# Kernel optimization log

Measured on AMD Instinct MI355X. Metric: run time of the kernel, lower is better.

Reference implementation:

```python
import jax, jax.numpy as jnp
import numpy as np

EPS = 1e-5

def prelu(x, a):
    return jnp.where(x >= 0, x, a * x)

def batch_norm(x, axes):
    # training-mode BatchNorm with gamma=1, beta=0 (init values)
    m = jnp.mean(x, axis=axes, keepdims=True)
    v = jnp.var(x, axis=axes, keepdims=True)
    return (x - m) / jnp.sqrt(v + EPS)

def conv_branch(X, w, b):
    # X: [B,N,F]; Conv2d(1,1,(1,k)) over the feature axis, VALID
    lhs = X[:, None, :, :]                      # [B,1,N,F]
    rhs = w.reshape(1, 1, 1, -1)                # OIHW
    out = jax.lax.conv_general_dilated(lhs, rhs, (1, 1), 'VALID',
        dimension_numbers=('NCHW', 'OIHW', 'NCHW'))
    return out[:, 0] + b                        # [B,N,F-k+1]

def setup_inputs() -> dict:
    key = jax.random.key(0)
    ks = jax.random.split(key, 16)
    B, N, F, H, D = 8192, 29, 147, 4, 128
    d_cat = 429
    s = 0.05
    return {
        'X': jax.random.normal(ks[0], (B, N, F), jnp.float32),
        'corr': jax.random.uniform(ks[1], (B, N, N), jnp.float32),
        'w_c1': s * jax.random.normal(ks[2], (3,), jnp.float32),
        'b_c1': jnp.zeros((1,), jnp.float32),
        'w_c2': s * jax.random.normal(ks[3], (5,), jnp.float32),
        'b_c2': jnp.zeros((1,), jnp.float32),
        'w_c3': s * jax.random.normal(ks[4], (7,), jnp.float32),
        'b_c3': jnp.zeros((1,), jnp.float32),
        'a_cnn': 0.25 * jnp.ones((1,), jnp.float32),
        'Wg': s * jax.random.normal(ks[5], (d_cat, D), jnp.float32),
        'bg': jnp.zeros((D,), jnp.float32),
        'a_gnn': 0.25 * jnp.ones((1,), jnp.float32),
        'centroids': jax.random.normal(ks[6], (H, 1, D), jnp.float32),
        'head_w': s * jax.random.normal(ks[7], (H,), jnp.float32),
        'Wp': s * jax.random.normal(ks[8], (D, D), jnp.float32),
        'bp': jnp.zeros((D,), jnp.float32),
        'Wm1': s * jax.random.normal(ks[9], (D, D), jnp.float32),
        'bm1': jnp.zeros((D,), jnp.float32),
        'a_mlp': 0.25 * jnp.ones((1,), jnp.float32),
        'Wm2': s * jax.random.normal(ks[10], (D, 1), jnp.float32),
        'bm2': jnp.zeros((1,), jnp.float32),
    }

def reference(X, corr, w_c1, b_c1, w_c2, b_c2, w_c3, b_c3, a_cnn,
              Wg, bg, a_gnn, centroids, head_w, Wp, bp,
              Wm1, bm1, a_mlp, Wm2, bm2):
    # three conv branches + concat + PReLU + BN over node channels
    a1 = conv_branch(X, w_c1, b_c1)             # [B,29,145]
    a2 = conv_branch(X, w_c2, b_c2)             # [B,29,143]
    a3 = conv_branch(X, w_c3, b_c3)             # [B,29,141]
    x = prelu(jnp.concatenate([a1, a2, a3], axis=2), a_cnn)  # [B,29,429]
    x = batch_norm(x, (0, 2))
    # GraphConv: A x W + b
    x = jnp.einsum('bnm,bmd->bnd', corr, x) @ Wg + bg        # [B,29,128]
    x = prelu(x, a_gnn)
    x = batch_norm(x, (0, 2))
    # CoSimPool: multi-head cosine-sim attention assignment to 1 cluster
    xn = x / (jnp.linalg.norm(x, axis=-1, keepdims=True) + 1e-8)
    cn = centroids / (jnp.linalg.norm(centroids, axis=-1, keepdims=True) + 1e-8)
    sim = jnp.einsum('hmd,bnd->bhmn', cn, xn)                # [B,4,1,29]
    agg = jnp.einsum('h,bhmn->bmn', head_w, sim)             # 1x1 conv over heads
    C = jax.nn.softmax(agg, axis=-1)                         # [B,1,29]
    x = jnp.einsum('bmn,bnd->bmd', C, x) @ Wp + bp           # [B,1,128]
    x = x[:, 0]                                              # squeeze(1)
    x = batch_norm(x, (0,))
    h = prelu(x @ Wm1 + bm1, a_mlp)
    y = jax.nn.sigmoid(h @ Wm2 + bm2)                        # [B,1]
    return y
```

## Files before the change

### kernel.cpp

```cpp
#include <hip/hip_runtime.h>

#define B_    8192
#define N_    29
#define F_    147
#define DC    429
#define D_    128
#define ROWS  (B_*N_)
#define EPSBN 1e-5f

#define UTSTR   4096
#define RS_SH   3712

#define X3_OFF   16777216
#define ACC_OFF  (X3_OFF + B_*D_)
#define BN1_OFF  (ACC_OFF)
#define BN2_OFF  (ACC_OFF + 1856)
#define BN3_OFF  (ACC_OFF + 3712)
#define FIN_OFF  (ACC_OFF + 11904)
#define M1_OFF   (FIN_OFF + 0)
#define IS1_OFF  (FIN_OFF + 32)
#define M2_OFF   (FIN_OFF + 64)
#define IS2_OFF  (FIN_OFF + 96)
#define M3_OFF   (FIN_OFF + 128)
#define IS3_OFF  (FIN_OFF + 256)
#define CSW_OFF  (FIN_OFF + 384)
#define V_OFF    (FIN_OFF + 512)
#define V1_OFF   (FIN_OFF + 640)
#define IMG_OFF  (FIN_OFF + 1024)

typedef __bf16 bf16x8 __attribute__((ext_vector_type(8)));
typedef float  f32x4  __attribute__((ext_vector_type(4)));

__device__ __forceinline__ unsigned short f2bf(float f) {
  unsigned int u = __float_as_uint(f);
  u += 0x7fffu + ((u >> 16) & 1u);
  return (unsigned short)(u >> 16);
}
__device__ __forceinline__ float bf2f(unsigned u16) {
  return __uint_as_float(u16 << 16);
}

#define TSTR 456
#define UTILS 34

__global__ void k0a_img(const float* __restrict__ Wg, float* __restrict__ ws)
{
  __shared__ float cs_l[8];
  const int tid = threadIdx.x;
  const int kb = blockIdx.x * 8;
  if (tid < 8) cs_l[tid] = 0.f;
  __syncthreads();
  unsigned short* img = (unsigned short*)(ws + IMG_OFF);
  for (int i = tid; i < 8*448; i += 256) {
    int kk = i / 448, dk = i - kk*448;
    int k = kb + kk;
    int d;
    if      (dk < 145)  d = dk;
    else if (dk == 145) d = -1;
    else if (dk < 289)  d = dk - 1;
    else if (dk == 289) d = -1;
    else if (dk < 431)  d = dk - 2;
    else                d = -1;
    float v = (d >= 0) ? Wg[(size_t)d*D_ + k] : 0.f;
    img[(size_t)k*448 + dk] = f2bf(v);
    if (d >= 0) atomicAdd(&cs_l[kk], v);
  }
  __syncthreads();
  if (tid < 8) ws[CSW_OFF + kb + tid] = cs_l[tid];
}

__global__ void k0b_cent(const float* __restrict__ cent, const float* __restrict__ hw,
                         float* __restrict__ ws)
{
  __shared__ float sq[128];
  __shared__ float nrm;
  const int tid = threadIdx.x;
  float vk = 0.f;
  for (int h = 0; h < 4; ++h) {
    float c = cent[h*D_ + tid];
    sq[tid] = c*c;
    __syncthreads();
    if (tid == 0) { float s=0.f; for (int j=0;j<128;++j) s+=sq[j]; nrm = sqrtf(s)+1e-8f; }
    __syncthreads();
    vk += hw[h] * c / nrm;
    __syncthreads();
  }
  ws[V_OFF + tid] = vk;
  sq[tid] = vk;
  __syncthreads();
  if (tid == 0) { float s=0.f; for (int j=0;j<128;++j) s+=sq[j]; ws[V1_OFF] = s; }
}

__global__ __launch_bounds__(512, 4) void k1_conv_gemm(
    const float* __restrict__ X,
    const float* __restrict__ wc1, const float* __restrict__ bc1,
    const float* __restrict__ wc2, const float* __restrict__ bc2,
    const float* __restrict__ wc3, const float* __restrict__ bc3,
    const float* __restrict__ acnn, float* __restrict__ ws)
{
  __shared__ unsigned short t_s[32*TSTR];
  __shared__ __align__(16) float xs[4272];
  const int tid = threadIdx.x;
  const int b = blockIdx.x;

  for (int i = tid; i < 3*456; i += 512) t_s[29*TSTR + i] = 0;
  for (int i = tid; i < 29*19; i += 512) {
    int r = i / 19, j = i - r*19;
    int col = (j == 0) ? 145 : ((j == 1) ? 289 : (429 + j));
    t_s[r*TSTR + col] = 0;
  }

  const float c10 = wc1[0], c11 = wc1[1], c12 = wc1[2], b1 = bc1[0];
  const float c20 = wc2[0], c21 = wc2[1], c22 = wc2[2], c23 = wc2[3], c24 = wc2[4], b2 = bc2[0];
  const float c30 = wc3[0], c31 = wc3[1], c32 = wc3[2], c33 = wc3[3], c34 = wc3[4],
              c35 = wc3[5], c36 = wc3[6], b3 = bc3[0];
  const float ap = acnn[0];

  {
    const float* xsrc = X + (size_t)b * N_ * F_;
    for (int i = tid; i < N_*F_; i += 512) xs[i] = xsrc[i];
  }
  __syncthreads();

  {
    const int r = tid >> 4, q = tid & 15;
    const int f0 = q * 10;
    float s1 = 0.f, s2 = 0.f;
    if (r < N_ && q < 15) {
      const int cnt = min(10, 145 - f0);
      const int n2 = min(cnt, 143 - f0);
      const int n3 = min(cnt, 141 - f0);
      const float* xr = xs + r*F_;
      unsigned short* tr = t_s + r*TSTR;
      unsigned int* tr32 = (unsigned int*)tr;
      float wA=xr[f0],wB=xr[f0+1],wC=xr[f0+2],wD=xr[f0+3],wE=xr[f0+4],wF=xr[f0+5],wG;
      float o1[10], o2[10], o3[10];
      #pragma unroll
      for (int i2 = 0; i2 < 10; ++i2) {
        if (i2 < cnt) {
          int f = f0 + i2;
          wG = (f + 6 < F_) ? xr[f+6] : 0.f;
          float v1 = fmaf(wA,c10, fmaf(wB,c11, fmaf(wC,c12, b1)));
          v1 = (v1 >= 0.f) ? v1 : ap*v1;
          float v2 = fmaf(wA,c20, fmaf(wB,c21, fmaf(wC,c22, fmaf(wD,c23, fmaf(wE,c24, b2)))));
          v2 = (v2 >= 0.f) ? v2 : ap*v2;
          float v3 = fmaf(wA,c30, fmaf(wB,c31, fmaf(wC,c32, fmaf(wD,c33, fmaf(wE,c34, fmaf(wF,c35, fmaf(wG,c36, b3)))))));
          v3 = (v3 >= 0.f) ? v3 : ap*v3;
          o1[i2] = v1; o2[i2] = v2; o3[i2] = v3;
          s1 += v1; s2 = fmaf(v1, v1, s2);
          if (i2 < n2) { s1 += v2; s2 = fmaf(v2, v2, s2); }
          if (i2 < n3) { s1 += v3; s2 = fmaf(v3, v3, s2); }
          wA=wB; wB=wC; wC=wD; wD=wE; wE=wF; wF=wG;
        }
      }
      #pragma unroll
      for (int i2 = 0; i2 < 10; i2 += 2) {
        if (i2+1 < cnt)     tr32[(f0+i2)>>1] = (unsigned)f2bf(o1[i2]) | ((unsigned)f2bf(o1[i2+1])<<16);
        else if (i2 < cnt)  tr[f0+i2] = f2bf(o1[i2]);
        if (i2+1 < n2)      tr32[(146+f0+i2)>>1] = (unsigned)f2bf(o2[i2]) | ((unsigned)f2bf(o2[i2+1])<<16);
        else if (i2 < n2)   tr[146+f0+i2] = f2bf(o2[i2]);
        if (i2+1 < n3)      tr32[(290+f0+i2)>>1] = (unsigned)f2bf(o3[i2]) | ((unsigned)f2bf(o3[i2+1])<<16);
        else if (i2 < n3)   tr[290+f0+i2] = f2bf(o3[i2]);
      }
    }
    #pragma unroll
    for (int off = 8; off >= 1; off >>= 1) {
      s1 += __shfl_xor(s1, off);
      s2 += __shfl_xor(s2, off);
    }
    if (r < N_ && q == 0) {
      float* bn1 = ws + BN1_OFF + (size_t)(b & 31) * 58;
      atomicAdd(&bn1[r*2+0], s1);
      atomicAdd(&bn1[r*2+1], s2);
    }
  }

  const int wv = tid >> 6, lane = tid & 63;
  const int lrow = lane & 15, quad = lane >> 4;
  const int n0 = wv * 16;
  const unsigned short* imgp = (const unsigned short*)(ws + IMG_OFF);
  const unsigned short* gB = imgp + (size_t)(n0 + lrow)*448 + quad*8;
  bf16x8 Bf[14];
  #pragma unroll
  for (int ks = 0; ks < 14; ++ks) Bf[ks] = *(const bf16x8*)(gB + ks*32);

  __syncthreads();

  f32x4 acc0 = (f32x4){0.f,0.f,0.f,0.f};
  f32x4 acc1 = (f32x4){0.f,0.f,0.f,0.f};
  #pragma unroll
  for (int ks = 0; ks < 14; ++ks) {
    const int k0 = ks * 32;
    bf16x8 A0 = *(const bf16x8*)&t_s[(lrow)*TSTR      + k0 + quad*8];
    bf16x8 A1 = *(const bf16x8*)&t_s[(16 + lrow)*TSTR + k0 + quad*8];
    acc0 = __builtin_amdgcn_mfma_f32_16x16x32_bf16(A0, Bf[ks], acc0, 0, 0, 0);
    acc1 = __builtin_amdgcn_mfma_f32_16x16x32_bf16(A1, Bf[ks], acc1, 0, 0, 0);
  }

  __syncthreads();
  unsigned short* utile = (unsigned short*)xs;
  {
    const int f = n0 + lrow;
    #pragma unroll
    for (int i = 0; i < 4; ++i) {
      utile[f*UTILS + quad*4 + i]      = f2bf(acc0[i]);
      utile[f*UTILS + 16 + quad*4 + i] = f2bf(acc1[i]);
    }
  }
  __syncthreads();
  {
    unsigned* Ug = (unsigned*)((unsigned short*)ws + (size_t)b * UTSTR);
    const unsigned* u32t = (const unsigned*)utile;
    #pragma unroll
    for (int it = 0; it < 4; ++it) {
      int idx = tid + it*512;
      int f = idx >> 4, pr = idx & 15;
      Ug[f*16 + pr] = u32t[f*17 + pr];
    }
  }
}

__global__ void k2_bn1(float* __restrict__ ws) {
  const int k = threadIdx.x;
  if (k < 29) {
    float s1 = 0.f, s2 = 0.f;
    for (int s = 0; s < 32; ++s) {
      s1 += ws[BN1_OFF + s*58 + k*2 + 0];
      s2 += ws[BN1_OFF + s*58 + k*2 + 1];
    }
    const float inv = 1.f / (float)(B_ * DC);
    float mean = s1 * inv;
    float var  = s2 * inv - mean * mean;
    ws[M1_OFF  + k] = mean;
    ws[IS1_OFF + k] = rsqrtf(var + EPSBN);
  }
}

__global__ __launch_bounds__(256) void k3_gnn(
    const float* __restrict__ corr, const float* __restrict__ bg,
    const float* __restrict__ agnn, float* __restrict__ ws)
{
  __shared__ float cwf[841];
  __shared__ unsigned short a_s[32*40];
  __shared__ float m1s[29], is1s[29], cms[29], st1s[29], st2s[29], svs[29];

  const int b = blockIdx.x, tid = threadIdx.x;
  const int wv = tid >> 6, lane = tid & 63;
  const int lrow = lane & 15, quad = lane >> 4;
  unsigned short* Utb = (unsigned short*)ws + (size_t)b * UTSTR;

  if (tid < 29) {
    m1s[tid] = ws[M1_OFF+tid]; is1s[tid] = ws[IS1_OFF+tid];
    st1s[tid] = 0.f; st2s[tid] = 0.f; svs[tid] = 0.f;
  }
  const float* cb = corr + (size_t)b * 841;
  for (int i = tid; i < 841; i += 256) cwf[i] = cb[i];
  __syncthreads();

  const int f0 = wv * 32;
  bf16x8 B0 = *(const bf16x8*)&Utb[(f0      + lrow)*32 + quad*8];
  bf16x8 B1 = *(const bf16x8*)&Utb[(f0 + 16 + lrow)*32 + quad*8];

  for (int i = tid; i < 1024; i += 256) {
    int n = i >> 5, m = i & 31;
    float v = (n < 29 && m < 29) ? cwf[n*29 + m] * is1s[m] : 0.f;
    a_s[n*40 + m] = f2bf(v);
  }
  if (tid < 29) {
    float cm = 0.f;
    for (int m = 0; m < 29; ++m) cm = fmaf(cwf[tid*29 + m] * is1s[m], m1s[m], cm);
    cms[tid] = cm;
  }
  __syncthreads();

  bf16x8 A0 = *(const bf16x8*)&a_s[lrow*40 + quad*8];
  bf16x8 A1 = *(const bf16x8*)&a_s[(16 + lrow)*40 + quad*8];
  f32x4 acc[2][2];
  acc[0][0] = (f32x4){0.f,0.f,0.f,0.f}; acc[0][1] = (f32x4){0.f,0.f,0.f,0.f};
  acc[1][0] = (f32x4){0.f,0.f,0.f,0.f}; acc[1][1] = (f32x4){0.f,0.f,0.f,0.f};
  acc[0][0] = __builtin_amdgcn_mfma_f32_16x16x32_bf16(A0, B0, acc[0][0], 0, 0, 0);
  acc[0][1] = __builtin_amdgcn_mfma_f32_16x16x32_bf16(A0, B1, acc[0][1], 0, 0, 0);
  acc[1][0] = __builtin_amdgcn_mfma_f32_16x16x32_bf16(A1, B0, acc[1][0], 0, 0, 0);
  acc[1][1] = __builtin_amdgcn_mfma_f32_16x16x32_bf16(A1, B1, acc[1][1], 0, 0, 0);
  __syncthreads();

  const float ag = agnn[0];
  const float vA  = ws[V_OFF  + f0 + lrow],      vB  = ws[V_OFF  + f0 + 16 + lrow];
  const float csA = ws[CSW_OFF + f0 + lrow],     csB = ws[CSW_OFF + f0 + 16 + lrow];
  const float bgA = bg[f0 + lrow],               bgB = bg[f0 + 16 + lrow];
  #pragma unroll
  for (int mt = 0; mt < 2; ++mt) {
    #pragma unroll
    for (int i = 0; i < 4; ++i) {
      int n = mt*16 + quad*4 + i;
      if (n < 29) {
        float y0 = acc[mt][0][i] - cms[n]*csA + bgA;
        float y1 = acc[mt][1][i] - cms[n]*csB + bgB;
        y0 = (y0 >= 0.f) ? y0 : ag*y0;
        y1 = (y1 >= 0.f) ? y1 : ag*y1;
        Utb[n*D_ + f0 + lrow]      = f2bf(y0);
        Utb[n*D_ + f0 + 16 + lrow] = f2bf(y1);
        float sy  = y0 + y1;
        float sy2 = fmaf(y0, y0, y1*y1);
        float sv  = fmaf(y0, vA, y1*vB);
        #pragma unroll
        for (int off = 8; off >= 1; off >>= 1) {
          sy  += __shfl_xor(sy, off);
          sy2 += __shfl_xor(sy2, off);
          sv  += __shfl_xor(sv, off);
        }
        if (lrow == 0) {
          atomicAdd(&st1s[n], sy);
          atomicAdd(&st2s[n], sy2);
          atomicAdd(&svs[n],  sv);
        }
      }
    }
  }
  __syncthreads();
  if (tid < 29) {
    float* rs = (float*)(Utb + RS_SH);
    rs[tid]      = st1s[tid];
    rs[29 + tid] = st2s[tid];
    rs[58 + tid] = svs[tid];
    float* bn2 = ws + BN2_OFF + (size_t)(b & 31) * 58;
    atomicAdd(&bn2[tid*2+0], st1s[tid]);
    atomicAdd(&bn2[tid*2+1], st2s[tid]);
  }
}

__global__ void k3_finalize2(float* __restrict__ ws) {
  const int n = threadIdx.x;
  if (n < 29) {
    float s1 = 0.f, s2 = 0.f;
    for (int s = 0; s < 32; ++s) {
      s1 += ws[BN2_OFF + s*58 + n*2 + 0];
      s2 += ws[BN2_OFF + s*58 + n*2 + 1];
    }
    const float inv = 1.f / (float)(B_ * D_);
    float mean = s1 * inv, var = s2 * inv - mean * mean;
    ws[M2_OFF + n] = mean;
    ws[IS2_OFF + n] = rsqrtf(var + EPSBN);
  }
}

__global__ __launch_bounds__(256) void k4_pool(
    const float* __restrict__ Wp, const float* __restrict__ bpv,
    float* __restrict__ ws)
{
  __shared__ float cs_s[4*32];
  __shared__ float pool_s[4*128];
  const int tid = threadIdx.x, wv = tid >> 6, lane = tid & 63;
  const int b = blockIdx.x * 4 + wv;
  const unsigned short* yb = (const unsigned short*)ws + (size_t)b * UTSTR;
  const float* rs = (const float*)(yb + RS_SH);
  const float V1 = ws[V1_OFF];

  float agg = -1e30f, m2 = 0.f, is2 = 0.f;
  if (lane < 29) {
    float S1 = rs[lane], S2 = rs[29+lane], Sv = rs[58+lane];
    m2 = ws[M2_OFF + lane]; is2 = ws[IS2_OFF + lane];
    float ss = fmaxf(S2 - 2.f*m2*S1 + 128.f*m2*m2, 0.f);
    float rn = sqrtf(ss);
    agg = (is2*(Sv - m2*V1)) / (is2*rn + 1e-8f);
  }
  float mx = agg;
  #pragma unroll
  for (int off = 32; off >= 1; off >>= 1) mx = fmaxf(mx, __shfl_xor(mx, off));
  float e = (lane < 29) ? __expf(agg - mx) : 0.f;
  float den = e, kof = e*is2*m2;
  #pragma unroll
  for (int off = 32; off >= 1; off >>= 1) { den += __shfl_xor(den, off); kof += __shfl_xor(kof, off); }
  float rden = 1.f / den;
  float koff = kof * rden;
  if (lane < 32) cs_s[wv*32 + lane] = (lane < 29) ? e*is2*rden : 0.f;
  __syncthreads();

  const unsigned* y32 = (const unsigned*)yb;
  float p0 = -koff, p1 = -koff;
  #pragma unroll
  for (int n = 0; n < 29; ++n) {
    float c = cs_s[wv*32 + n];
    unsigned u = y32[n*64 + lane];
    p0 = fmaf(c, bf2f(u & 0xffffu), p0);
    p1 = fmaf(c, bf2f(u >> 16), p1);
  }
  pool_s[wv*128 + 2*lane]     = p0;
  pool_s[wv*128 + 2*lane + 1] = p1;
  __syncthreads();

  float a0 = bpv[lane], a1 = bpv[64 + lane];
  const float* ps = pool_s + wv*128;
  #pragma unroll 4
  for (int j = 0; j < 128; ++j) {
    float p = ps[j];
    a0 = fmaf(p, Wp[j*D_ + lane], a0);
    a1 = fmaf(p, Wp[j*D_ + 64 + lane], a1);
  }
  ws[X3_OFF + (size_t)b*D_ + lane]      = a0;
  ws[X3_OFF + (size_t)b*D_ + 64 + lane] = a1;
  float* bn3 = ws + BN3_OFF + (size_t)(b & 31) * 256;
  atomicAdd(&bn3[lane*2+0], a0);
  atomicAdd(&bn3[lane*2+1], a0*a0);
  atomicAdd(&bn3[(64+lane)*2+0], a1);
  atomicAdd(&bn3[(64+lane)*2+1], a1*a1);
}

__global__ void k4_finalize3(float* __restrict__ ws) {
  const int k = threadIdx.x;
  float s1 = 0.f, s2 = 0.f;
  for (int s = 0; s < 32; ++s) {
    s1 += ws[BN3_OFF + s*256 + k*2 + 0];
    s2 += ws[BN3_OFF + s*256 + k*2 + 1];
  }
  const float inv = 1.f / (float)B_;
  float mean = s1 * inv, var = s2 * inv - mean * mean;
  ws[M3_OFF + k] = mean;
  ws[IS3_OFF + k] = rsqrtf(var + EPSBN);
}

__global__ __launch_bounds__(128) void k5_mlp(
    const float* __restrict__ Wm1, const float* __restrict__ bm1,
    const float* __restrict__ amlp, const float* __restrict__ Wm2,
    const float* __restrict__ bm2, const float* __restrict__ ws,
    float* __restrict__ out)
{
  __shared__ float x_s[128];
  __shared__ float red[2];
  const int b = blockIdx.x, k = threadIdx.x;
  float x = (ws[X3_OFF + (size_t)b*D_ + k] - ws[M3_OFF + k]) * ws[IS3_OFF + k];
  x_s[k] = x;
  __syncthreads();
  float h = bm1[k];
  #pragma unroll 4
  for (int j = 0; j < 128; ++j) h = fmaf(x_s[j], Wm1[j*D_ + k], h);
  const float am = amlp[0];
  h = (h >= 0.f) ? h : am * h;
  float rr = h * Wm2[k];
  #pragma unroll
  for (int off = 32; off >= 1; off >>= 1) rr += __shfl_down(rr, off);
  if ((k & 63) == 0) red[k >> 6] = rr;
  __syncthreads();
  if (k == 0) {
    float logit = red[0] + red[1] + bm2[0];
    out[b] = 1.f / (1.f + expf(-logit));
  }
}

extern "C" void kernel_launch(void* const* d_in, const int* in_sizes, int n_in,
                              void* d_out, int out_size, void* d_ws, size_t ws_size,
                              hipStream_t stream)
{
  (void)in_sizes; (void)n_in; (void)out_size; (void)ws_size;
  const float* X    = (const float*)d_in[0];
  const float* corr = (const float*)d_in[1];
  const float* wc1  = (const float*)d_in[2];
  const float* bc1  = (const float*)d_in[3];
  const float* wc2  = (const float*)d_in[4];
  const float* bc2  = (const float*)d_in[5];
  const float* wc3  = (const float*)d_in[6];
  const float* bc3  = (const float*)d_in[7];
  const float* acnn = (const float*)d_in[8];
  const float* Wg   = (const float*)d_in[9];
  const float* bg   = (const float*)d_in[10];
  const float* agnn = (const float*)d_in[11];
  const float* cent = (const float*)d_in[12];
  const float* hw   = (const float*)d_in[13];
  const float* Wp   = (const float*)d_in[14];
  const float* bp   = (const float*)d_in[15];
  const float* Wm1  = (const float*)d_in[16];
  const float* bm1  = (const float*)d_in[17];
  const float* amlp = (const float*)d_in[18];
  const float* Wm2  = (const float*)d_in[19];
  const float* bm2  = (const float*)d_in[20];
  float* ws  = (float*)d_ws;
  float* out = (float*)d_out;

  hipMemsetAsync(ws + ACC_OFF, 0, 11904 * sizeof(float), stream);
  k0a_img<<<16, 256, 0, stream>>>(Wg, ws);
  k0b_cent<<<1, 128, 0, stream>>>(cent, hw, ws);
  k1_conv_gemm<<<B_, 512, 0, stream>>>(X, wc1, bc1, wc2, bc2, wc3, bc3, acnn, ws);
  k2_bn1<<<1, 32, 0, stream>>>(ws);
  k3_gnn<<<B_, 256, 0, stream>>>(corr, bg, agnn, ws);
  k3_finalize2<<<1, 32, 0, stream>>>(ws);
  k4_pool<<<B_/4, 256, 0, stream>>>(Wp, bp, ws);
  k4_finalize3<<<1, 128, 0, stream>>>(ws);
  k5_mlp<<<B_, 128, 0, stream>>>(Wm1, bm1, amlp, Wm2, bm2, ws, out);
}
```

Measured before the change: 530.5 us.

## Process two batches per conv-GEMM block and four rows per MLP block

k1_conv_gemm now handles two batch elements per 512-thread block. It reads X directly from global memory instead of staging it in shared memory, and each wave computes a 32x32 output tile with four MFMAs. The B fragments are prefetched one k-step ahead rather than all held in registers, and the conv writes become scalar bf16 stores. k5_mlp handles four batch rows per block so each Wm1 load is reused four times. The aim is to cut block count and launch overhead and improve weight reuse, at the cost of lower occupancy (launch bounds 2), uncoalesced strided X reads, and narrower shared-memory stores.

```diff
diff --git a/kernel.cpp b/kernel.cpp
--- a/kernel.cpp
+++ b/kernel.cpp
@@ -91,23 +91,27 @@
   if (tid == 0) { float s=0.f; for (int j=0;j<128;++j) s+=sq[j]; ws[V1_OFF] = s; }
 }
 
-__global__ __launch_bounds__(512, 4) void k1_conv_gemm(
+__global__ __launch_bounds__(512, 2) void k1_conv_gemm(
     const float* __restrict__ X,
     const float* __restrict__ wc1, const float* __restrict__ bc1,
     const float* __restrict__ wc2, const float* __restrict__ bc2,
     const float* __restrict__ wc3, const float* __restrict__ bc3,
     const float* __restrict__ acnn, float* __restrict__ ws)
 {
-  __shared__ unsigned short t_s[32*TSTR];
-  __shared__ __align__(16) float xs[4272];
+  __shared__ __align__(16) unsigned short t_s[64*TSTR];
   const int tid = threadIdx.x;
-  const int b = blockIdx.x;
-
-  for (int i = tid; i < 3*456; i += 512) t_s[29*TSTR + i] = 0;
-  for (int i = tid; i < 29*19; i += 512) {
-    int r = i / 19, j = i - r*19;
+  const int b0 = blockIdx.x * 2;
+
+  for (int i = tid; i < 2*3*448; i += 512) {
+    int bb = i / (3*448), rem = i - bb*(3*448);
+    int r = rem / 448, c = rem - r*448;
+    t_s[(bb*32 + 29 + r)*TSTR + c] = 0;
+  }
+  for (int i = tid; i < 58*19; i += 512) {
+    int rr = i / 19, j = i - rr*19;
+    int bb = (rr >= 29), n = rr - bb*29;
     int col = (j == 0) ? 145 : ((j == 1) ? 289 : (429 + j));
-    t_s[r*TSTR + col] = 0;
+    t_s[(bb*32 + n)*TSTR + col] = 0;
   }
 
   const float c10 = wc1[0], c11 = wc1[1], c12 = wc1[2], b1 = bc1[0];
@@ -117,105 +121,108 @@
   const float ap = acnn[0];
 
   {
-    const float* xsrc = X + (size_t)b * N_ * F_;
-    for (int i = tid; i < N_*F_; i += 512) xs[i] = xsrc[i];
-  }
-  __syncthreads();
-
-  {
-    const int r = tid >> 4, q = tid & 15;
-    const int f0 = q * 10;
+    const int r = tid >> 3, q = tid & 7;
+    const int bb = r >> 5, n = r & 31;
+    const int f0 = q * 19;
     float s1 = 0.f, s2 = 0.f;
-    if (r < N_ && q < 15) {
-      const int cnt = min(10, 145 - f0);
+    const bool act = (n < 29);
+    if (act) {
+      const int cnt = min(19, 145 - f0);
       const int n2 = min(cnt, 143 - f0);
       const int n3 = min(cnt, 141 - f0);
-      const float* xr = xs + r*F_;
-      unsigned short* tr = t_s + r*TSTR;
-      unsigned int* tr32 = (unsigned int*)tr;
+      const float* xr = X + (size_t)((b0 + bb)*N_ + n) * F_;
+      unsigned short* tr = t_s + (bb*32 + n)*TSTR;
       float wA=xr[f0],wB=xr[f0+1],wC=xr[f0+2],wD=xr[f0+3],wE=xr[f0+4],wF=xr[f0+5],wG;
-      float o1[10], o2[10], o3[10];
       #pragma unroll
-      for (int i2 = 0; i2 < 10; ++i2) {
+      for (int i2 = 0; i2 < 19; ++i2) {
         if (i2 < cnt) {
           int f = f0 + i2;
           wG = (f + 6 < F_) ? xr[f+6] : 0.f;
           float v1 = fmaf(wA,c10, fmaf(wB,c11, fmaf(wC,c12, b1)));
           v1 = (v1 >= 0.f) ? v1 : ap*v1;
-          float v2 = fmaf(wA,c20, fmaf(wB,c21, fmaf(wC,c22, fmaf(wD,c23, fmaf(wE,c24, b2)))));
-          v2 = (v2 >= 0.f) ? v2 : ap*v2;
-          float v3 = fmaf(wA,c30, fmaf(wB,c31, fmaf(wC,c32, fmaf(wD,c33, fmaf(wE,c34, fmaf(wF,c35, fmaf(wG,c36, b3)))))));
-          v3 = (v3 >= 0.f) ? v3 : ap*v3;
-          o1[i2] = v1; o2[i2] = v2; o3[i2] = v3;
           s1 += v1; s2 = fmaf(v1, v1, s2);
-          if (i2 < n2) { s1 += v2; s2 = fmaf(v2, v2, s2); }
-          if (i2 < n3) { s1 += v3; s2 = fmaf(v3, v3, s2); }
+          tr[f] = f2bf(v1);
+          if (i2 < n2) {
+            float v2 = fmaf(wA,c20, fmaf(wB,c21, fmaf(wC,c22, fmaf(wD,c23, fmaf(wE,c24, b2)))));
+            v2 = (v2 >= 0.f) ? v2 : ap*v2;
+            s1 += v2; s2 = fmaf(v2, v2, s2);
+            tr[146+f] = f2bf(v2);
+          }
+          if (i2 < n3) {
+            float v3 = fmaf(wA,c30, fmaf(wB,c31, fmaf(wC,c32, fmaf(wD,c33, fmaf(wE,c34, fmaf(wF,c35, fmaf(wG,c36, b3)))))));
+            v3 = (v3 >= 0.f) ? v3 : ap*v3;
+            s1 += v3; s2 = fmaf(v3, v3, s2);
+            tr[290+f] = f2bf(v3);
+          }
           wA=wB; wB=wC; wC=wD; wD=wE; wE=wF; wF=wG;
         }
       }
-      #pragma unroll
-      for (int i2 = 0; i2 < 10; i2 += 2) {
-        if (i2+1 < cnt)     tr32[(f0+i2)>>1] = (unsigned)f2bf(o1[i2]) | ((unsigned)f2bf(o1[i2+1])<<16);
-        else if (i2 < cnt)  tr[f0+i2] = f2bf(o1[i2]);
-        if (i2+1 < n2)      tr32[(146+f0+i2)>>1] = (unsigned)f2bf(o2[i2]) | ((unsigned)f2bf(o2[i2+1])<<16);
-        else if (i2 < n2)   tr[146+f0+i2] = f2bf(o2[i2]);
-        if (i2+1 < n3)      tr32[(290+f0+i2)>>1] = (unsigned)f2bf(o3[i2]) | ((unsigned)f2bf(o3[i2+1])<<16);
-        else if (i2 < n3)   tr[290+f0+i2] = f2bf(o3[i2]);
-      }
     }
     #pragma unroll
-    for (int off = 8; off >= 1; off >>= 1) {
+    for (int off = 4; off >= 1; off >>= 1) {
       s1 += __shfl_xor(s1, off);
       s2 += __shfl_xor(s2, off);
     }
-    if (r < N_ && q == 0) {
-      float* bn1 = ws + BN1_OFF + (size_t)(b & 31) * 58;
-      atomicAdd(&bn1[r*2+0], s1);
-      atomicAdd(&bn1[r*2+1], s2);
-    }
-  }
+    if (act && q == 0) {
+      float* bn1 = ws + BN1_OFF + (size_t)(blockIdx.x & 31) * 58;
+      atomicAdd(&bn1[n*2+0], s1);
+      atomicAdd(&bn1[n*2+1], s2);
+    }
+  }
+  __syncthreads();
 
   const int wv = tid >> 6, lane = tid & 63;
   const int lrow = lane & 15, quad = lane >> 4;
-  const int n0 = wv * 16;
+  const int bb = wv >> 2;
+  const int n0 = (wv & 3) * 32;
   const unsigned short* imgp = (const unsigned short*)(ws + IMG_OFF);
-  const unsigned short* gB = imgp + (size_t)(n0 + lrow)*448 + quad*8;
-  bf16x8 Bf[14];
-  #pragma unroll
-  for (int ks = 0; ks < 14; ++ks) Bf[ks] = *(const bf16x8*)(gB + ks*32);
-
-  __syncthreads();
-
-  f32x4 acc0 = (f32x4){0.f,0.f,0.f,0.f};
-  f32x4 acc1 = (f32x4){0.f,0.f,0.f,0.f};
+  const unsigned short* gB0 = imgp + (size_t)(n0 + lrow)*448 + quad*8;
+  const unsigned short* gB1 = gB0 + 16*448;
+  const unsigned short* tA = t_s + (size_t)(bb*32)*TSTR + quad*8;
+
+  f32x4 a00 = (f32x4){0.f,0.f,0.f,0.f}, a01 = a00, a10 = a00, a11 = a00;
+  bf16x8 Bc0 = *(const bf16x8*)(gB0);
+  bf16x8 Bc1 = *(const bf16x8*)(gB1);
   #pragma unroll
   for (int ks = 0; ks < 14; ++ks) {
-    const int k0 = ks * 32;
-    bf16x8 A0 = *(const bf16x8*)&t_s[(lrow)*TSTR      + k0 + quad*8];
-    bf16x8 A1 = *(const bf16x8*)&t_s[(16 + lrow)*TSTR + k0 + quad*8];
-    acc0 = __builtin_amdgcn_mfma_f32_16x16x32_bf16(A0, Bf[ks], acc0, 0, 0, 0);
-    acc1 = __builtin_amdgcn_mfma_f32_16x16x32_bf16(A1, Bf[ks], acc1, 0, 0, 0);
-  }
-
-  __syncthreads();
-  unsigned short* utile = (unsigned short*)xs;
+    bf16x8 Bn0, Bn1;
+    if (ks < 13) {
+      Bn0 = *(const bf16x8*)(gB0 + (ks+1)*32);
+      Bn1 = *(const bf16x8*)(gB1 + (ks+1)*32);
+    }
+    bf16x8 A0 = *(const bf16x8*)(tA + lrow*TSTR + ks*32);
+    bf16x8 A1 = *(const bf16x8*)(tA + (16+lrow)*TSTR + ks*32);
+    a00 = __builtin_amdgcn_mfma_f32_16x16x32_bf16(A0, Bc0, a00, 0, 0, 0);
+    a01 = __builtin_amdgcn_mfma_f32_16x16x32_bf16(A0, Bc1, a01, 0, 0, 0);
+    a10 = __builtin_amdgcn_mfma_f32_16x16x32_bf16(A1, Bc0, a10, 0, 0, 0);
+    a11 = __builtin_amdgcn_mfma_f32_16x16x32_bf16(A1, Bc1, a11, 0, 0, 0);
+    Bc0 = Bn0; Bc1 = Bn1;
+  }
+  __syncthreads();
+
   {
-    const int f = n0 + lrow;
+    unsigned short* ut = t_s + bb*4352;
+    const int fb0 = n0 + lrow, fb1 = n0 + 16 + lrow;
     #pragma unroll
     for (int i = 0; i < 4; ++i) {
-      utile[f*UTILS + quad*4 + i]      = f2bf(acc0[i]);
-      utile[f*UTILS + 16 + quad*4 + i] = f2bf(acc1[i]);
+      int m0 = quad*4 + i, m1 = 16 + quad*4 + i;
+      ut[fb0*UTILS + m0] = f2bf(a00[i]);
+      ut[fb1*UTILS + m0] = f2bf(a01[i]);
+      ut[fb0*UTILS + m1] = f2bf(a10[i]);
+      ut[fb1*UTILS + m1] = f2bf(a11[i]);
     }
   }
   __syncthreads();
   {
-    unsigned* Ug = (unsigned*)((unsigned short*)ws + (size_t)b * UTSTR);
-    const unsigned* u32t = (const unsigned*)utile;
+    const unsigned* u32t = (const unsigned*)t_s;
+    unsigned short* ws16 = (unsigned short*)ws;
     #pragma unroll
-    for (int it = 0; it < 4; ++it) {
+    for (int it = 0; it < 8; ++it) {
       int idx = tid + it*512;
-      int f = idx >> 4, pr = idx & 15;
-      Ug[f*16 + pr] = u32t[f*17 + pr];
+      int bbs = idx >> 11, rem = idx & 2047;
+      int f = rem >> 4, pr = rem & 15;
+      unsigned* Ug = (unsigned*)(ws16 + (size_t)(b0 + bbs)*UTSTR);
+      Ug[f*16 + pr] = u32t[bbs*2176 + f*17 + pr];
     }
   }
 }
@@ -425,25 +432,44 @@
     const float* __restrict__ bm2, const float* __restrict__ ws,
     float* __restrict__ out)
 {
-  __shared__ float x_s[128];
-  __shared__ float red[2];
-  const int b = blockIdx.x, k = threadIdx.x;
-  float x = (ws[X3_OFF + (size_t)b*D_ + k] - ws[M3_OFF + k]) * ws[IS3_OFF + k];
-  x_s[k] = x;
-  __syncthreads();
-  float h = bm1[k];
+  __shared__ float x_s[4*128];
+  __shared__ float red[4][2];
+  const int b0 = blockIdx.x * 4, k = threadIdx.x;
+  const float m3 = ws[M3_OFF + k], is3 = ws[IS3_OFF + k];
+  #pragma unroll
+  for (int bb = 0; bb < 4; ++bb)
+    x_s[bb*128 + k] = (ws[X3_OFF + (size_t)(b0+bb)*D_ + k] - m3) * is3;
+  __syncthreads();
+  float h0 = bm1[k], h1 = h0, h2 = h0, h3 = h0;
   #pragma unroll 4
-  for (int j = 0; j < 128; ++j) h = fmaf(x_s[j], Wm1[j*D_ + k], h);
+  for (int j = 0; j < 128; ++j) {
+    float w = Wm1[j*D_ + k];
+    h0 = fmaf(x_s[j],       w, h0);
+    h1 = fmaf(x_s[128 + j], w, h1);
+    h2 = fmaf(x_s[256 + j], w, h2);
+    h3 = fmaf(x_s[384 + j], w, h3);
+  }
   const float am = amlp[0];
-  h = (h >= 0.f) ? h : am * h;
-  float rr = h * Wm2[k];
-  #pragma unroll
-  for (int off = 32; off >= 1; off >>= 1) rr += __shfl_down(rr, off);
-  if ((k & 63) == 0) red[k >> 6] = rr;
-  __syncthreads();
-  if (k == 0) {
-    float logit = red[0] + red[1] + bm2[0];
-    out[b] = 1.f / (1.f + expf(-logit));
+  const float w2 = Wm2[k];
+  h0 = ((h0 >= 0.f) ? h0 : am*h0) * w2;
+  h1 = ((h1 >= 0.f) ? h1 : am*h1) * w2;
+  h2 = ((h2 >= 0.f) ? h2 : am*h2) * w2;
+  h3 = ((h3 >= 0.f) ? h3 : am*h3) * w2;
+  #pragma unroll
+  for (int off = 32; off >= 1; off >>= 1) {
+    h0 += __shfl_down(h0, off);
+    h1 += __shfl_down(h1, off);
+    h2 += __shfl_down(h2, off);
+    h3 += __shfl_down(h3, off);
+  }
+  if ((k & 63) == 0) {
+    int w = k >> 6;
+    red[0][w] = h0; red[1][w] = h1; red[2][w] = h2; red[3][w] = h3;
+  }
+  __syncthreads();
+  if (k < 4) {
+    float logit = red[k][0] + red[k][1] + bm2[0];
+    out[b0 + k] = 1.f / (1.f + expf(-logit));
   }
 }
 
@@ -479,11 +505,11 @@
   hipMemsetAsync(ws + ACC_OFF, 0, 11904 * sizeof(float), stream);
   k0a_img<<<16, 256, 0, stream>>>(Wg, ws);
   k0b_cent<<<1, 128, 0, stream>>>(cent, hw, ws);
-  k1_conv_gemm<<<B_, 512, 0, stream>>>(X, wc1, bc1, wc2, bc2, wc3, bc3, acnn, ws);
+  k1_conv_gemm<<<B_/2, 512, 0, stream>>>(X, wc1, bc1, wc2, bc2, wc3, bc3, acnn, ws);
   k2_bn1<<<1, 32, 0, stream>>>(ws);
   k3_gnn<<<B_, 256, 0, stream>>>(corr, bg, agnn, ws);
   k3_finalize2<<<1, 32, 0, stream>>>(ws);
   k4_pool<<<B_/4, 256, 0, stream>>>(Wp, bp, ws);
   k4_finalize3<<<1, 128, 0, stream>>>(ws);
-  k5_mlp<<<B_, 128, 0, stream>>>(Wm1, bm1, amlp, Wm2, bm2, ws, out);
-}
+  k5_mlp<<<B_/4, 128, 0, stream>>>(Wm1, bm1, amlp, Wm2, bm2, ws, out);
+}
```

Result: faster. 492.7 us (-7.1%).
